# Optimization experiments

Measured on AMD Instinct MI355X. Metric: run time of the kernel, lower is better.

## Reference

```python
import jax, jax.numpy as jnp
import numpy as np
from jax.scipy.special import gammaln, xlogy

B, N, DIM, H, DK, DV = 2, 2048, 1536, 8, 64, 64
NRPF = 192  # num_rel_pos_features, already divisible by 6


def get_positional_embed(n, feat):
    # Enformer positional basis: exponential, central-mask, gamma; then sign-antisymmetrized.
    nb = feat // 6  # num basis per class
    d = jnp.arange(-n + 1, n, dtype=jnp.float32)          # [2n-1]
    ad = jnp.abs(d)[:, None]                              # [2n-1, 1]
    # exponential decay features
    max_range = np.log(n) / np.log(2.0)
    half_life = 2.0 ** jnp.linspace(3.0, max_range, nb)
    e = jnp.exp(-np.log(2.0) / half_life * ad)
    # central mask features
    widths = 2.0 ** jnp.arange(1, nb + 1, dtype=jnp.float32) - 1.0
    c = (widths > ad).astype(jnp.float32)
    # gamma pdf features
    std = n / (2.0 * nb)
    mean = jnp.linspace(n / nb, float(n), nb)
    conc = (mean / std) ** 2
    rate = mean / (std ** 2)
    logp = xlogy(conc - 1.0, ad) - rate * ad - (gammaln(conc) - conc * jnp.log(rate))
    p = jnp.exp(logp) + 1e-8
    g = p / jnp.max(p)
    emb = jnp.concatenate([e, c, g], axis=-1)             # [2n-1, feat//2]
    return jnp.concatenate([emb, jnp.sign(d)[:, None] * emb], axis=-1)  # [2n-1, feat]


def relative_shift(x):
    # x: [b, h, i, 2i-1] -> [b, h, i, i]
    b, h, i, j = x.shape
    x = jnp.pad(x, ((0, 0), (0, 0), (0, 0), (1, 0)))      # [b,h,i,j+1]
    x = x.reshape(b, h, j + 1, i)[:, :, 1:, :]            # drop first 'row'
    x = x.reshape(b, h, i, j)
    return x[..., : (j + 2) // 2]                          # keep first i cols


def setup_inputs() -> dict:
    key = jax.random.key(0)
    ks = jax.random.split(key, 9)
    s = 0.02
    return {
        "x": jax.random.normal(ks[0], (B, N, DIM), jnp.float32),
        "Wq": jax.random.normal(ks[1], (DIM, H * DK), jnp.float32) * s,
        "Wk": jax.random.normal(ks[2], (DIM, H * DK), jnp.float32) * s,
        "Wv": jax.random.normal(ks[3], (DIM, H * DV), jnp.float32) * s,
        "Wo": jax.random.normal(ks[4], (H * DV, DIM), jnp.float32) * s,
        "bo": jnp.zeros((DIM,), jnp.float32),
        "Wrel": jax.random.normal(ks[5], (NRPF, H * DK), jnp.float32) * s,
        "rel_content_bias": jax.random.normal(ks[6], (1, H, 1, DK), jnp.float32),
        "rel_pos_bias": jax.random.normal(ks[7], (1, H, 1, DK), jnp.float32),
    }


def reference(x, Wq, Wk, Wv, Wo, bo, Wrel, rel_content_bias, rel_pos_bias):
    b, n, _ = x.shape
    scale = DK ** -0.5
    split = lambda t, d: t.reshape(b, n, H, d).transpose(0, 2, 1, 3)  # b h n d
    q = split(x @ Wq, DK) * scale
    k = split(x @ Wk, DK)
    v = split(x @ Wv, DV)
    content_logits = jnp.einsum('bhid,bhjd->bhij', q + rel_content_bias, k)
    pos = get_positional_embed(n, NRPF) @ Wrel               # [2n-1, H*DK]
    pos = pos.reshape(2 * n - 1, H, DK).transpose(1, 0, 2)   # h j d
    rel_logits = jnp.einsum('bhid,hjd->bhij', q + rel_pos_bias, pos)
    rel_logits = relative_shift(rel_logits)
    attn = jax.nn.softmax(content_logits + rel_logits, axis=-1)
    out = jnp.einsum('bhij,bhjd->bhid', attn, v)
    out = out.transpose(0, 2, 1, 3).reshape(b, n, H * DV)
    return out @ Wo + bo
```

## Files before the change

### kernel.cpp

```cpp
#include <hip/hip_runtime.h>
#include <stdint.h>
#include <cmath>

#define B_    2
#define N_    2048
#define DIM_  1536
#define H_    8
#define NPOS  (2*N_ - 1)
#define NB_   32

typedef __attribute__((ext_vector_type(8))) short short8;
typedef __attribute__((ext_vector_type(4))) float float4v;

struct PosConsts {
    float  inv_hl[32];
    int    widthI[32];
    float  c1[32];
    float  rateF[32];
    double gc[32];
    double maxp;
};

__device__ __forceinline__ float bf2f(unsigned short u) {
    return __uint_as_float(((unsigned int)u) << 16);
}
__device__ __forceinline__ unsigned short f2bf(float f) {
    unsigned int u = __float_as_uint(f);
    u += 0x7FFFu + ((u >> 16) & 1u);
    return (unsigned short)(u >> 16);
}
__device__ __forceinline__ unsigned int cvtpk(float lo, float hi) {
    unsigned int r;
    asm("v_cvt_pk_bf16_f32 %0, %1, %2" : "=v"(r) : "v"(lo), "v"(hi));
    return r;
}
__device__ __forceinline__ unsigned int pack2bf(float lo, float hi) {
    return cvtpk(lo, hi);
}
__device__ __forceinline__ float ldf(const void* p, int isF32, size_t idx) {
    return isF32 ? ((const float*)p)[idx] : bf2f(((const unsigned short*)p)[idx]);
}
__device__ __forceinline__ void gll16(const unsigned short* g, unsigned short* l) {
    __builtin_amdgcn_global_load_lds(
        (const __attribute__((address_space(1))) unsigned int*)g,
        (__attribute__((address_space(3))) unsigned int*)l, 16, 0, 0);
}

constexpr size_t OFF_FLAG = 0;
constexpr size_t OFF_POS  = 256;
constexpr size_t OFF_Q    = OFF_POS + (size_t)H_*4096*64*2;
constexpr size_t OFF_K    = OFF_Q   + (size_t)B_*H_*N_*64*2;
constexpr size_t OFF_V    = OFF_K   + (size_t)B_*H_*N_*64*2;
constexpr size_t OFF_WOT  = OFF_V   + (size_t)B_*H_*N_*64*2;
constexpr size_t OFF_XB   = OFF_WOT + (size_t)DIM_*512*2;
constexpr size_t OFF_AO   = OFF_XB;
constexpr size_t OFF_OP   = OFF_AO + (size_t)4096*512*2;
constexpr size_t OFF_LP   = OFF_OP + (size_t)3*16*32*4096*2;
constexpr size_t OFF_WT   = OFF_XB + (size_t)4096*DIM_*2;
static_assert(OFF_LP + (size_t)3*16*32*64*4 <= OFF_WT + (size_t)3*512*DIM_*2, "ws overflow");

__global__ __launch_bounds__(512) void prep_kernel(PosConsts pc,
                                                   const void* __restrict__ x,
                                                   const void* __restrict__ Wq, const void* __restrict__ Wk,
                                                   const void* __restrict__ Wv, const void* __restrict__ Wo,
                                                   const void* __restrict__ Wrel,
                                                   unsigned int* __restrict__ flags,
                                                   unsigned short* __restrict__ Xb,
                                                   unsigned short* __restrict__ Wt,
                                                   unsigned short* __restrict__ Wot,
                                                   unsigned short* __restrict__ posb) {
    __shared__ __align__(16) char smraw[16 * 192 * 4];
    const int tid = threadIdx.x;
    const int bid = blockIdx.x;

    int* cnt = (int*)smraw;
    int ok = 0;
    if (tid < 256) {
        unsigned short u = ((const unsigned short*)x)[2 * tid];
        int e = (u >> 7) & 0xFF;
        ok = (u == 0) || (e >= 95 && e <= 140);
    }
    cnt[tid] = ok;
    __syncthreads();
    for (int s = 256; s > 0; s >>= 1) {
        if (tid < s) cnt[tid] += cnt[tid + s];
        __syncthreads();
    }
    const int f32 = !(cnt[0] >= 192);
    __syncthreads();
    if (bid == 0 && tid == 0) flags[0] = (unsigned int)f32;

    if (bid < 256) {
        float* eb = (float*)smraw;
        const int j0 = bid * 16;
        const int c  = tid;
        for (int u = c; u < 16 * 96; u += 512) {
            int rr = u / 96, f = u - rr * 96;
            int j = j0 + rr;
            float v = 0.f, sg = 0.f;
            if (j < NPOS) {
                int dd  = j - (N_ - 1);
                int adI = dd < 0 ? -dd : dd;
                float val;
                if (f < 32) {
                    val = exp2f(-(float)adI * pc.inv_hl[f]);
                } else if (f < 64) {
                    val = (adI < pc.widthI[f - 32]) ? 1.f : 0.f;
                } else {
                    int g = f - 64;
                    if (adI == 0) {
                        val = (float)(1e-8 / pc.maxp);
                    } else {
                        double lp = (double)pc.c1[g] * log((double)adI)
                                  - (double)pc.rateF[g] * (double)adI + pc.gc[g];
                        double p = (double)expf((float)lp) + 1e-8;
                        val = (float)(p / pc.maxp);
                    }
                }
                v  = val;
                sg = (dd > 0) ? 1.f : ((dd < 0) ? -1.f : 0.f);
            }
            eb[rr * 192 + f]      = v;
            eb[rr * 192 + 96 + f] = sg * v;
        }
        __syncthreads();
        float acc[16];
#pragma unroll
        for (int rr = 0; rr < 16; ++rr) acc[rr] = 0.f;
        for (int k = 0; k < 192; k += 4) {
            float w0 = ldf(Wrel, f32, (size_t)(k + 0) * 512 + c);
            float w1 = ldf(Wrel, f32, (size_t)(k + 1) * 512 + c);
            float w2 = ldf(Wrel, f32, (size_t)(k + 2) * 512 + c);
            float w3 = ldf(Wrel, f32, (size_t)(k + 3) * 512 + c);
#pragma unroll
            for (int rr = 0; rr < 16; ++rr) {
                float4v e = *reinterpret_cast<const float4v*>(&eb[rr * 192 + k]);
                acc[rr] += e[0] * w0;
                acc[rr] += e[1] * w1;
                acc[rr] += e[2] * w2;
                acc[rr] += e[3] * w3;
            }
        }
        int h = c >> 6, dcol = c & 63;
#pragma unroll
        for (int rr = 0; rr < 16; ++rr) {
            int j = j0 + rr;
            if (j < NPOS)
                posb[((size_t)h * 4096 + j) * 64 + dcol] = f2bf(acc[rr]);
        }
    } else if (bid < 3328) {
        unsigned short (*tile)[33] = (unsigned short(*)[33])smraw;
        const int idx = bid - 256;
        const int z = idx / 768, rem = idx % 768;
        const int bx = rem & 15, by = rem >> 4;
        const void* src = z == 0 ? Wq : (z == 1 ? Wk : (z == 2 ? Wv : Wo));
        unsigned short* dst = (z < 3) ? (Wt + (size_t)z * 512 * DIM_) : Wot;
        const int R = (z < 3) ? DIM_ : 512;
        const int C = (z < 3) ? 512 : DIM_;
        const int x0 = ((z < 3) ? bx : by) * 32;
        const int y0 = ((z < 3) ? by : bx) * 32;
        const int tx = tid & 31, ty = tid >> 5;
#pragma unroll
        for (int i = 0; i < 2; ++i)
            tile[ty + i * 16][tx] = f2bf(ldf(src, f32, (size_t)(y0 + ty + i * 16) * C + x0 + tx));
        __syncthreads();
#pragma unroll
        for (int i = 0; i < 2; ++i)
            dst[(size_t)(x0 + ty + i * 16) * R + y0 + tx] = tile[tx][ty + i * 16];
    } else {
        const int ab = bid - 3328;
        const size_t total = (size_t)4096 * DIM_;
        size_t i = ((size_t)ab * 512 + tid) * 8;
        const size_t stride = (size_t)1024 * 512 * 8;
        if (f32) {
            for (; i < total; i += stride) {
                float4v a = *reinterpret_cast<const float4v*>((const float*)x + i);
                float4v b = *reinterpret_cast<const float4v*>((const float*)x + i + 4);
                uint4 o;
                o.x = pack2bf(a[0], a[1]); o.y = pack2bf(a[2], a[3]);
                o.z = pack2bf(b[0], b[1]); o.w = pack2bf(b[2], b[3]);
                *reinterpret_cast<uint4*>(Xb + i) = o;
            }
        } else {
            for (; i < total; i += stride)
                *reinterpret_cast<uint4*>(Xb + i) =
                    *reinterpret_cast<const uint4*>((const unsigned short*)x + i);
        }
    }
}

__device__ __forceinline__ void gemm128_core(const unsigned short* __restrict__ A,
                                             const unsigned short* __restrict__ Bt,
                                             int K, int row0, int col0,
                                             unsigned short* As, unsigned short* Bs,
                                             float4v acc[4][4]) {
    const int tid = threadIdx.x, lane = tid & 63, w = tid >> 6;
    const int l15 = lane & 15, q8 = (lane >> 4) * 8;
    const int mr0 = (w >> 1) * 64, nc0 = (w & 1) * 64;
    const int sr = lane >> 2, sc8 = (lane & 3) * 8;
    for (int k0 = 0; k0 < K; k0 += 32) {
        __syncthreads();
        gll16(&A [(size_t)(row0 + w * 32 + sr) * K + k0 + sc8],      &As[w * 1024]);
        gll16(&A [(size_t)(row0 + w * 32 + 16 + sr) * K + k0 + sc8], &As[w * 1024 + 512]);
        gll16(&Bt[(size_t)(col0 + w * 32 + sr) * K + k0 + sc8],      &Bs[w * 1024]);
        gll16(&Bt[(size_t)(col0 + w * 32 + 16 + sr) * K + k0 + sc8], &Bs[w * 1024 + 512]);
        __syncthreads();
        short8 a[4], b[4];
#pragma unroll
        for (int mi = 0; mi < 4; ++mi)
            a[mi] = *reinterpret_cast<const short8*>(&As[(mr0 + mi * 16 + l15) * 32 + q8]);
#pragma unroll
        for (int ni = 0; ni < 4; ++ni)
            b[ni] = *reinterpret_cast<const short8*>(&Bs[(nc0 + ni * 16 + l15) * 32 + q8]);
#pragma unroll
        for (int mi = 0; mi < 4; ++mi)
#pragma unroll
            for (int ni = 0; ni < 4; ++ni)
                acc[mi][ni] = __builtin_amdgcn_mfma_f32_16x16x32_bf16(a[mi], b[ni], acc[mi][ni], 0, 0, 0);
    }
}

__global__ __launch_bounds__(256) void qkv_kernel(const unsigned short* __restrict__ Xb,
                                                  const unsigned short* __restrict__ Wt,
                                                  unsigned short* __restrict__ qbuf,
                                                  unsigned short* __restrict__ kbuf,
                                                  unsigned short* __restrict__ vbuf) {
    __shared__ __align__(16) unsigned short As[128 * 32];
    __shared__ __align__(16) unsigned short Bs[128 * 32];
    const int row0 = blockIdx.y * 128, col0 = blockIdx.x * 128;
    float4v acc[4][4];
#pragma unroll
    for (int mi = 0; mi < 4; ++mi)
#pragma unroll
        for (int ni = 0; ni < 4; ++ni) acc[mi][ni] = (float4v){0.f, 0.f, 0.f, 0.f};
    gemm128_core(Xb, Wt, DIM_, row0, col0, As, Bs, acc);
    const int lane = threadIdx.x & 63, w = threadIdx.x >> 6;
    const int l15 = lane & 15, quad = lane >> 4;
    const int mr0 = (w >> 1) * 64, nc0 = (w & 1) * 64;
#pragma unroll
    for (int mi = 0; mi < 4; ++mi)
#pragma unroll
        for (int ni = 0; ni < 4; ++ni) {
            int n = col0 + nc0 + ni * 16 + l15;
            int mode = n >> 9, nn = n & 511;
            int hh = nn >> 6, dd = nn & 63;
            int mb = row0 + mr0 + mi * 16 + quad * 4;
            int bb = mb >> 11, ii = mb & 2047;
            if (mode == 2) {
                union { unsigned short us[4]; uint2 u2; } pk;
                unsigned int p0 = cvtpk(acc[mi][ni][0], acc[mi][ni][1]);
                unsigned int p1 = cvtpk(acc[mi][ni][2], acc[mi][ni][3]);
                pk.u2 = (uint2){p0, p1};
                *reinterpret_cast<uint2*>(
                    &vbuf[((size_t)(bb * 8 + hh) * 64 + dd) * 2048 + ii]) = pk.u2;
            } else {
                unsigned short* Obuf = (mode == 0) ? qbuf : kbuf;
                float scale = (mode == 0) ? 0.125f : 1.0f;
#pragma unroll
                for (int r = 0; r < 4; ++r)
                    Obuf[((size_t)(bb * 8 + hh) * N_ + ii + r) * 64 + dd] = f2bf(acc[mi][ni][r] * scale);
            }
        }
}

#define SLD 72
#define RST 68

__device__ __forceinline__ void stage64(const unsigned short* __restrict__ g,
                                        unsigned short* __restrict__ s, int tid) {
    int r = tid >> 2, d0 = (tid & 3) * 16;
    const uint4* p = reinterpret_cast<const uint4*>(g + (size_t)r * 64 + d0);
    *reinterpret_cast<uint4*>(&s[r * SLD + d0])     = p[0];
    *reinterpret_cast<uint4*>(&s[r * SLD + d0 + 8]) = p[1];
}

__global__ __launch_bounds__(256) void attn_kernel(const unsigned int* __restrict__ flags,
                                                   const unsigned short* __restrict__ qb,
                                                   const unsigned short* __restrict__ kb,
                                                   const unsigned short* __restrict__ vb,
                                                   const unsigned short* __restrict__ posb,
                                                   const void* __restrict__ rcb,
                                                   const void* __restrict__ rpb,
                                                   unsigned short* __restrict__ Opart,
                                                   float* __restrict__ lpart) {
    __shared__ __align__(16) unsigned short Ks[64 * SLD];
    __shared__ __align__(16) unsigned short Ps[64 * SLD];
    __shared__ __align__(16) unsigned short Vt[64 * SLD];
    __shared__ __align__(16) unsigned short Pp[64 * SLD];
    __shared__ __align__(8)  unsigned short Rb[128 * RST];

    const int f32 = (int)flags[0];
    const int tid = threadIdx.x;
    const int it = blockIdx.x, bh = blockIdx.y, z = blockIdx.z;
    const int h = bh & 7;
    const int i0 = it * 64;
    const size_t qoff = (size_t)bh * N_ * 64;
    const size_t voff = (size_t)bh * 64 * 2048;
    const size_t poff = (size_t)h * 4096 * 64;
    const int lane = tid & 63, w = tid >> 6;
    const int l15 = lane & 15, quad = lane >> 4, q8 = quad * 8;
    const int m0 = w * 16 + quad * 4;
    const int sr = tid >> 2, sc = (tid & 3) * 16;

    short8 afc[2], afr[2];
#pragma unroll
    for (int kc = 0; kc < 2; ++kc) {
        uint4 qv = *reinterpret_cast<const uint4*>(
            &qb[qoff + (size_t)(i0 + w * 16 + l15) * 64 + kc * 32 + q8]);
        unsigned int uu[4] = {qv.x, qv.y, qv.z, qv.w};
        unsigned int cw[4], rw[4];
#pragma unroll
        for (int e = 0; e < 4; ++e) {
            int k = h * 64 + kc * 32 + q8 + 2 * e;
            float lo = __uint_as_float(uu[e] << 16);
            float hi = __uint_as_float(uu[e] & 0xffff0000u);
            cw[e] = pack2bf(lo + ldf(rcb, f32, k), hi + ldf(rcb, f32, k + 1));
            rw[e] = pack2bf(lo + ldf(rpb, f32, k), hi + ldf(rpb, f32, k + 1));
        }
        union { uint4 u; short8 s; } cv, rv2;
        cv.u  = (uint4){cw[0], cw[1], cw[2], cw[3]};
        rv2.u = (uint4){rw[0], rw[1], rw[2], rw[3]};
        afc[kc] = cv.s;
        afr[kc] = rv2.s;
    }

    float4v Oa[4];
#pragma unroll
    for (int nb = 0; nb < 4; ++nb) Oa[nb] = (float4v){0.f, 0.f, 0.f, 0.f};
    float lsum[4] = {0.f, 0.f, 0.f, 0.f};

    const int base0 = 1984 - i0;
    const int t0 = z * 11, t1 = (z == 2) ? 32 : (t0 + 11);
    const int cs0 = base0 + t0 * 64;

    stage64(&posb[poff + (size_t)cs0 * 64], Ps, tid);
    __syncthreads();
    {
        float4v R[4];
#pragma unroll
        for (int nb = 0; nb < 4; ++nb) R[nb] = (float4v){0.f, 0.f, 0.f, 0.f};
        __builtin_amdgcn_s_setprio(1);
#pragma unroll
        for (int kc = 0; kc < 2; ++kc)
#pragma unroll
            for (int nb = 0; nb < 4; ++nb) {
                short8 pb = *reinterpret_cast<const short8*>(&Ps[(nb * 16 + l15) * SLD + kc * 32 + q8]);
                R[nb] = __builtin_amdgcn_mfma_f32_16x16x32_bf16(afr[kc], pb, R[nb], 0, 0, 0);
            }
        __builtin_amdgcn_s_setprio(0);
#pragma unroll
        for (int nb = 0; nb < 4; ++nb) {
            int ta = cs0 + nb * 16 + l15;
            unsigned int pk0 = cvtpk(R[nb][0], R[nb][1]);
            unsigned int pk1 = cvtpk(R[nb][2], R[nb][3]);
            Rb[(size_t)((ta + m0 + 0) & 127) * RST + m0 + 0] = (unsigned short)pk0;
            Rb[(size_t)((ta + m0 + 1) & 127) * RST + m0 + 1] = (unsigned short)(pk0 >> 16);
            Rb[(size_t)((ta + m0 + 2) & 127) * RST + m0 + 2] = (unsigned short)pk1;
            Rb[(size_t)((ta + m0 + 3) & 127) * RST + m0 + 3] = (unsigned short)(pk1 >> 16);
        }
    }
    __syncthreads();

    stage64(&kb[qoff + (size_t)(t0 * 64) * 64], Ks, tid);
    stage64(&posb[poff + (size_t)(cs0 + 64) * 64], Ps, tid);
    {
        const unsigned short* gv = &vb[voff + (size_t)sr * 2048 + t0 * 64 + sc];
        *reinterpret_cast<uint4*>(&Vt[sr * SLD + sc])     = *reinterpret_cast<const uint4*>(gv);
        *reinterpret_cast<uint4*>(&Vt[sr * SLD + sc + 8]) = *reinterpret_cast<const uint4*>(gv + 8);
    }
    __syncthreads();

    for (int jt = t0; jt < t1; ++jt) {
        const int j0 = jt * 64, basej = base0 + j0;
        const bool hasn = (jt + 1 < t1);

        uint4 kr0, kr1, pr0, pr1, vr0, vr1;
        if (hasn) {
            const unsigned short* gk = &kb[qoff + (size_t)(j0 + 64 + sr) * 64 + sc];
            kr0 = *reinterpret_cast<const uint4*>(gk);
            kr1 = *reinterpret_cast<const uint4*>(gk + 8);
            const unsigned short* gp = &posb[poff + (size_t)(basej + 128 + sr) * 64 + sc];
            pr0 = *reinterpret_cast<const uint4*>(gp);
            pr1 = *reinterpret_cast<const uint4*>(gp + 8);
            const unsigned short* gv = &vb[voff + (size_t)sr * 2048 + j0 + 64 + sc];
            vr0 = *reinterpret_cast<const uint4*>(gv);
            vr1 = *reinterpret_cast<const uint4*>(gv + 8);
            __builtin_amdgcn_sched_barrier(0);
        }

        {
            float4v R[4];
#pragma unroll
            for (int nb = 0; nb < 4; ++nb) R[nb] = (float4v){0.f, 0.f, 0.f, 0.f};
            __builtin_amdgcn_s_setprio(1);
#pragma unroll
            for (int kc = 0; kc < 2; ++kc)
#pragma unroll
                for (int nb = 0; nb < 4; ++nb) {
                    short8 pb = *reinterpret_cast<const short8*>(&Ps[(nb * 16 + l15) * SLD + kc * 32 + q8]);
                    R[nb] = __builtin_amdgcn_mfma_f32_16x16x32_bf16(afr[kc], pb, R[nb], 0, 0, 0);
                }
            __builtin_amdgcn_s_setprio(0);
            const int tb = basej + 64;
#pragma unroll
            for (int nb = 0; nb < 4; ++nb) {
                int ta = tb + nb * 16 + l15;
                unsigned int pk0 = cvtpk(R[nb][0], R[nb][1]);
                unsigned int pk1 = cvtpk(R[nb][2], R[nb][3]);
                Rb[(size_t)((ta + m0 + 0) & 127) * RST + m0 + 0] = (unsigned short)pk0;
                Rb[(size_t)((ta + m0 + 1) & 127) * RST + m0 + 1] = (unsigned short)(pk0 >> 16);
                Rb[(size_t)((ta + m0 + 2) & 127) * RST + m0 + 2] = (unsigned short)pk1;
                Rb[(size_t)((ta + m0 + 3) & 127) * RST + m0 + 3] = (unsigned short)(pk1 >> 16);
            }
        }

        float4v Sacc[4];
#pragma unroll
        for (int nb = 0; nb < 4; ++nb) Sacc[nb] = (float4v){0.f, 0.f, 0.f, 0.f};
        __builtin_amdgcn_s_setprio(1);
#pragma unroll
        for (int kc = 0; kc < 2; ++kc)
#pragma unroll
            for (int nb = 0; nb < 4; ++nb) {
                short8 kf = *reinterpret_cast<const short8*>(&Ks[(nb * 16 + l15) * SLD + kc * 32 + q8]);
                Sacc[nb] = __builtin_amdgcn_mfma_f32_16x16x32_bf16(afc[kc], kf, Sacc[nb], 0, 0, 0);
            }
        __builtin_amdgcn_s_setprio(0);

        float pv4[4][4];
#pragma unroll
        for (int nb = 0; nb < 4; ++nb) {
            const int jl = nb * 16 + l15;
            const int row = (basej + 63 + jl) & 127;
            union { uint2 u2; unsigned short us[4]; } rv;
            rv.u2 = *reinterpret_cast<const uint2*>(&Rb[(size_t)row * RST + m0]);
#pragma unroll
            for (int r = 0; r < 4; ++r) {
                float p = __expf(Sacc[nb][r] + bf2f(rv.us[r]));
                pv4[nb][r] = p;
                lsum[r] += p;
            }
        }
#pragma unroll
        for (int r = 0; r < 4; ++r) {
            unsigned short* prow = &Pp[(m0 + r) * SLD + l15];
#pragma unroll
            for (int np = 0; np < 2; ++np) {
                unsigned int pk = cvtpk(pv4[2 * np][r], pv4[2 * np + 1][r]);
                prow[(2 * np) * 16]     = (unsigned short)pk;
                prow[(2 * np + 1) * 16] = (unsigned short)(pk >> 16);
            }
        }

        __builtin_amdgcn_s_setprio(1);
#pragma unroll
        for (int kc = 0; kc < 2; ++kc) {
            short8 pf = *reinterpret_cast<const short8*>(&Pp[(w * 16 + l15) * SLD + kc * 32 + q8]);
#pragma unroll
            for (int nb = 0; nb < 4; ++nb) {
                short8 vf = *reinterpret_cast<const short8*>(&Vt[(nb * 16 + l15) * SLD + kc * 32 + q8]);
                Oa[nb] = __builtin_amdgcn_mfma_f32_16x16x32_bf16(pf, vf, Oa[nb], 0, 0, 0);
            }
        }
        __builtin_amdgcn_s_setprio(0);

        if (hasn) {
            __syncthreads();
            *reinterpret_cast<uint4*>(&Ks[sr * SLD + sc])     = kr0;
            *reinterpret_cast<uint4*>(&Ks[sr * SLD + sc + 8]) = kr1;
            *reinterpret_cast<uint4*>(&Ps[sr * SLD + sc])     = pr0;
            *reinterpret_cast<uint4*>(&Ps[sr * SLD + sc + 8]) = pr1;
            *reinterpret_cast<uint4*>(&Vt[sr * SLD + sc])     = vr0;
            *reinterpret_cast<uint4*>(&Vt[sr * SLD + sc + 8]) = vr1;
            __syncthreads();
        }
    }

#pragma unroll
    for (int r = 0; r < 4; ++r)
#pragma unroll
        for (int off = 1; off < 16; off <<= 1) lsum[r] += __shfl_xor(lsum[r], off);
    const size_t pslot = (size_t)(z * 16 + bh) * 32 + it;
    const size_t obase = pslot * 4096;
#pragma unroll
    for (int nb = 0; nb < 4; ++nb) {
        unsigned int pk0 = cvtpk(Oa[nb][0], Oa[nb][1]);
        unsigned int pk1 = cvtpk(Oa[nb][2], Oa[nb][3]);
        unsigned short* prow = &Pp[m0 * SLD + nb * 16 + l15];
        prow[0 * SLD] = (unsigned short)pk0;
        prow[1 * SLD] = (unsigned short)(pk0 >> 16);
        prow[2 * SLD] = (unsigned short)pk1;
        prow[3 * SLD] = (unsigned short)(pk1 >> 16);
    }
    {
        const int rr2 = w * 16 + (lane >> 2), cc2 = (lane & 3) * 16;
        uint4 o0 = *reinterpret_cast<const uint4*>(&Pp[rr2 * SLD + cc2]);
        uint4 o1 = *reinterpret_cast<const uint4*>(&Pp[rr2 * SLD + cc2 + 8]);
        *reinterpret_cast<uint4*>(&Opart[obase + (size_t)rr2 * 64 + cc2])     = o0;
        *reinterpret_cast<uint4*>(&Opart[obase + (size_t)rr2 * 64 + cc2 + 8]) = o1;
    }
    if (l15 == 0) {
#pragma unroll
        for (int r = 0; r < 4; ++r) lpart[pslot * 64 + m0 + r] = lsum[r];
    }
}

__global__ __launch_bounds__(256) void combine_kernel(const unsigned short* __restrict__ Opart,
                                                      const float* __restrict__ lpart,
                                                      unsigned short* __restrict__ ao) {
    const int it = blockIdx.x, bh = blockIdx.y;
    const int h = bh & 7, b = bh >> 3, i0 = it * 64;
    const int tid = threadIdx.x;
    const int row = tid >> 2, c0 = (tid & 3) * 16;
    float o[16];
#pragma unroll
    for (int e = 0; e < 16; ++e) o[e] = 0.f;
    float l = 0.f;
#pragma unroll
    for (int z = 0; z < 3; ++z) {
        const size_t pslot = (size_t)(z * 16 + bh) * 32 + it;
        const size_t ob = pslot * 4096 + (size_t)row * 64 + c0;
        uint4 a = *reinterpret_cast<const uint4*>(&Opart[ob]);
        uint4 b4 = *reinterpret_cast<const uint4*>(&Opart[ob + 8]);
        unsigned int uu[8] = {a.x, a.y, a.z, a.w, b4.x, b4.y, b4.z, b4.w};
#pragma unroll
        for (int e = 0; e < 8; ++e) {
            o[2 * e]     += __uint_as_float(uu[e] << 16);
            o[2 * e + 1] += __uint_as_float(uu[e] & 0xffff0000u);
        }
        l += lpart[pslot * 64 + row];
    }
    float inv = 1.0f / l;
    unsigned int ou[8];
#pragma unroll
    for (int e = 0; e < 8; ++e) ou[e] = pack2bf(o[2 * e] * inv, o[2 * e + 1] * inv);
    unsigned short* dst = &ao[((size_t)b * N_ + i0 + row) * 512 + h * 64 + c0];
    *reinterpret_cast<uint4*>(dst)     = (uint4){ou[0], ou[1], ou[2], ou[3]};
    *reinterpret_cast<uint4*>(dst + 8) = (uint4){ou[4], ou[5], ou[6], ou[7]};
}

__global__ __launch_bounds__(256) void outproj_kernel(const unsigned int* __restrict__ flags,
                                                      const unsigned short* __restrict__ AO,
                                                      const unsigned short* __restrict__ Wot,
                                                      const void* __restrict__ bo,
                                                      void* __restrict__ out) {
    __shared__ __align__(16) unsigned short As[128 * 32];
    __shared__ __align__(16) unsigned short Bs[128 * 32];
    const int f32 = (int)flags[0];
    const int row0 = blockIdx.y * 128, col0 = blockIdx.x * 128;
    float4v acc[4][4];
#pragma unroll
    for (int mi = 0; mi < 4; ++mi)
#pragma unroll
        for (int ni = 0; ni < 4; ++ni) acc[mi][ni] = (float4v){0.f, 0.f, 0.f, 0.f};
    gemm128_core(AO, Wot, 512, row0, col0, As, Bs, acc);
    const int lane = threadIdx.x & 63, w = threadIdx.x >> 6;
    const int l15 = lane & 15, quad = lane >> 4;
    const int mr0 = (w >> 1) * 64, nc0 = (w & 1) * 64;
#pragma unroll
    for (int mi = 0; mi < 4; ++mi)
#pragma unroll
        for (int ni = 0; ni < 4; ++ni) {
            int n = col0 + nc0 + ni * 16 + l15;
            float bias = ldf(bo, f32, n);
#pragma unroll
            for (int r = 0; r < 4; ++r) {
                int m = row0 + mr0 + mi * 16 + quad * 4 + r;
                float v = acc[mi][ni][r] + bias;
                if (f32) ((float*)out)[(size_t)m * DIM_ + n] = v;
                else     ((unsigned short*)out)[(size_t)m * DIM_ + n] = f2bf(v);
            }
        }
}

extern "C" void kernel_launch(void* const* d_in, const int* in_sizes, int n_in,
                              void* d_out, int out_size, void* d_ws, size_t ws_size,
                              hipStream_t stream) {
    const void* x    = d_in[0];
    const void* Wq   = d_in[1];
    const void* Wk   = d_in[2];
    const void* Wv   = d_in[3];
    const void* Wo   = d_in[4];
    const void* bo   = d_in[5];
    const void* Wrel = d_in[6];
    const void* rcb  = d_in[7];
    const void* rpb  = d_in[8];

    char* ws = (char*)d_ws;
    unsigned int*   flags = (unsigned int*)(ws + OFF_FLAG);
    unsigned short* posb  = (unsigned short*)(ws + OFF_POS);
    unsigned short* qbuf  = (unsigned short*)(ws + OFF_Q);
    unsigned short* kbuf  = (unsigned short*)(ws + OFF_K);
    unsigned short* vbuf  = (unsigned short*)(ws + OFF_V);
    unsigned short* Wot   = (unsigned short*)(ws + OFF_WOT);
    unsigned short* Xb    = (unsigned short*)(ws + OFF_XB);
    unsigned short* ao    = (unsigned short*)(ws + OFF_AO);
    unsigned short* Opart = (unsigned short*)(ws + OFF_OP);
    float*          lpart = (float*)(ws + OFF_LP);
    unsigned short* Wt    = (unsigned short*)(ws + OFF_WT);

    PosConsts pc;
    double maxp = 0.0;
    for (int g = 0; g < NB_; ++g) {
        double mean = 64.0 * (g + 1);
        double conc = (mean / 32.0) * (mean / 32.0);
        double rate = mean / 1024.0;
        double lgc  = std::lgamma(conc);
        double clr  = conc * std::log(rate);
        for (int ad = 1; ad < N_; ++ad) {
            double lp = (conc - 1.0) * std::log((double)ad) - rate * (double)ad - lgc + clr;
            double p  = std::exp(lp) + 1e-8;
            if (p > maxp) maxp = p;
        }
        pc.c1[g]    = (float)(conc - 1.0);
        pc.rateF[g] = (float)rate;
        pc.gc[g]    = -lgc + clr;
    }
    pc.maxp = maxp;
    const double max_range = std::log((double)N_) / std::log(2.0);
    for (int f = 0; f < 32; ++f) {
        double t = 3.0 + (double)f * (max_range - 3.0) / 31.0;
        pc.inv_hl[f] = (float)std::exp2(-t);
        int e = f + 1;
        pc.widthI[f] = (e >= 12) ? 0x7FFFFFFF : ((1 << e) - 1);
    }

    prep_kernel<<<dim3(4352), dim3(512), 0, stream>>>(pc, x, Wq, Wk, Wv, Wo, Wrel,
                                                      flags, Xb, Wt, Wot, posb);
    qkv_kernel<<<dim3(12, 32), dim3(256), 0, stream>>>(Xb, Wt, qbuf, kbuf, vbuf);
    attn_kernel<<<dim3(32, 16, 3), dim3(256), 0, stream>>>(flags, qbuf, kbuf, vbuf, posb, rcb, rpb, Opart, lpart);
    combine_kernel<<<dim3(32, 16), dim3(256), 0, stream>>>(Opart, lpart, ao);
    outproj_kernel<<<dim3(12, 32), dim3(256), 0, stream>>>(flags, ao, Wot, bo, d_out);
}
```

Before: 263.4 us.

## Double-buffer attention K/pos/V tiles with direct global-to-LDS loads and XOR swizzle

Replaces the register-staged single-buffer K, positional and V tiles in the attention loop with double-buffered LDS tiles filled by direct global-to-LDS loads (gll16), prefetching the next tile while the current one is computed. The producers of K, V and the positional table now write in an XOR-swizzled layout, so the unpadded 64-wide LDS rows avoid bank conflicts when MFMA fragments are read. This removes one of the two barriers per iteration and the register round-trip, but doubles LDS use for these buffers. It also relies on gll16 ordering, with only one barrier per iteration ordering the async loads.

```diff
diff --git a/kernel.cpp b/kernel.cpp
--- a/kernel.cpp
+++ b/kernel.cpp
@@ -146,7 +146,7 @@
         for (int rr = 0; rr < 16; ++rr) {
             int j = j0 + rr;
             if (j < NPOS)
-                posb[((size_t)h * 4096 + j) * 64 + dcol] = f2bf(acc[rr]);
+                posb[((size_t)h * 4096 + j) * 64 + (dcol ^ ((j & 7) << 3))] = f2bf(acc[rr]);
         }
     } else if (bid < 3328) {
         unsigned short (*tile)[33] = (unsigned short(*)[33])smraw;
@@ -251,14 +251,20 @@
                 unsigned int p0 = cvtpk(acc[mi][ni][0], acc[mi][ni][1]);
                 unsigned int p1 = cvtpk(acc[mi][ni][2], acc[mi][ni][3]);
                 pk.u2 = (uint2){p0, p1};
+                int jb = (ii & ~63) | ((ii & 63) ^ ((dd & 7) << 3));
                 *reinterpret_cast<uint2*>(
-                    &vbuf[((size_t)(bb * 8 + hh) * 64 + dd) * 2048 + ii]) = pk.u2;
+                    &vbuf[((size_t)(bb * 8 + hh) * 64 + dd) * 2048 + jb]) = pk.u2;
+            } else if (mode == 1) {
+#pragma unroll
+                for (int r = 0; r < 4; ++r) {
+                    int tok = ii + r;
+                    kbuf[((size_t)(bb * 8 + hh) * N_ + tok) * 64 + (dd ^ ((tok & 7) << 3))]
+                        = f2bf(acc[mi][ni][r]);
+                }
             } else {
-                unsigned short* Obuf = (mode == 0) ? qbuf : kbuf;
-                float scale = (mode == 0) ? 0.125f : 1.0f;
 #pragma unroll
                 for (int r = 0; r < 4; ++r)
-                    Obuf[((size_t)(bb * 8 + hh) * N_ + ii + r) * 64 + dd] = f2bf(acc[mi][ni][r] * scale);
+                    qbuf[((size_t)(bb * 8 + hh) * N_ + ii + r) * 64 + dd] = f2bf(acc[mi][ni][r] * 0.125f);
             }
         }
 }
@@ -266,12 +272,21 @@
 #define SLD 72
 #define RST 68
 
-__device__ __forceinline__ void stage64(const unsigned short* __restrict__ g,
-                                        unsigned short* __restrict__ s, int tid) {
-    int r = tid >> 2, d0 = (tid & 3) * 16;
-    const uint4* p = reinterpret_cast<const uint4*>(g + (size_t)r * 64 + d0);
-    *reinterpret_cast<uint4*>(&s[r * SLD + d0])     = p[0];
-    *reinterpret_cast<uint4*>(&s[r * SLD + d0 + 8]) = p[1];
+__device__ __forceinline__ void stage_lin(const unsigned short* __restrict__ g,
+                                          unsigned short* s, int tid, int w) {
+    gll16(g + tid * 8,        s + w * 512);
+    gll16(g + 2048 + tid * 8, s + 2048 + w * 512);
+}
+__device__ __forceinline__ void stage_vt(const unsigned short* __restrict__ vbase,
+                                         int jbase, unsigned short* s, int tid, int w) {
+    {
+        int L = tid * 8;        int d = L >> 6, cb = L & 63;
+        gll16(vbase + (size_t)d * 2048 + jbase + cb, s + w * 512);
+    }
+    {
+        int L = 2048 + tid * 8; int d = L >> 6, cb = L & 63;
+        gll16(vbase + (size_t)d * 2048 + jbase + cb, s + 2048 + w * 512);
+    }
 }
 
 __global__ __launch_bounds__(256) void attn_kernel(const unsigned int* __restrict__ flags,
@@ -283,9 +298,9 @@
                                                    const void* __restrict__ rpb,
                                                    unsigned short* __restrict__ Opart,
                                                    float* __restrict__ lpart) {
-    __shared__ __align__(16) unsigned short Ks[64 * SLD];
-    __shared__ __align__(16) unsigned short Ps[64 * SLD];
-    __shared__ __align__(16) unsigned short Vt[64 * SLD];
+    __shared__ __align__(16) unsigned short Ks[2][4096];
+    __shared__ __align__(16) unsigned short Ps[2][4096];
+    __shared__ __align__(16) unsigned short Vt[2][4096];
     __shared__ __align__(16) unsigned short Pp[64 * SLD];
     __shared__ __align__(8)  unsigned short Rb[128 * RST];
 
@@ -295,12 +310,12 @@
     const int h = bh & 7;
     const int i0 = it * 64;
     const size_t qoff = (size_t)bh * N_ * 64;
-    const size_t voff = (size_t)bh * 64 * 2048;
     const size_t poff = (size_t)h * 4096 * 64;
+    const unsigned short* vbase = vb + (size_t)bh * 64 * 2048;
     const int lane = tid & 63, w = tid >> 6;
     const int l15 = lane & 15, quad = lane >> 4, q8 = quad * 8;
     const int m0 = w * 16 + quad * 4;
-    const int sr = tid >> 2, sc = (tid & 3) * 16;
+    const int swz = (l15 & 7) << 3;
 
     short8 afc[2], afr[2];
 #pragma unroll
@@ -331,9 +346,15 @@
 
     const int base0 = 1984 - i0;
     const int t0 = z * 11, t1 = (z == 2) ? 32 : (t0 + 11);
+    const int NT = t1 - t0;
     const int cs0 = base0 + t0 * 64;
 
-    stage64(&posb[poff + (size_t)cs0 * 64], Ps, tid);
+    {
+        int r = tid >> 2, c16 = (tid & 3) * 16;
+        const uint4* psrc = reinterpret_cast<const uint4*>(&posb[poff + (size_t)(cs0 + r) * 64 + c16]);
+        *reinterpret_cast<uint4*>(&Ps[0][r * 64 + c16])     = psrc[0];
+        *reinterpret_cast<uint4*>(&Ps[0][r * 64 + c16 + 8]) = psrc[1];
+    }
     __syncthreads();
     {
         float4v R[4];
@@ -344,7 +365,8 @@
         for (int kc = 0; kc < 2; ++kc)
 #pragma unroll
             for (int nb = 0; nb < 4; ++nb) {
-                short8 pb = *reinterpret_cast<const short8*>(&Ps[(nb * 16 + l15) * SLD + kc * 32 + q8]);
+                short8 pb = *reinterpret_cast<const short8*>(
+                    &Ps[0][(nb * 16 + l15) * 64 + ((kc * 32 + q8) ^ swz)]);
                 R[nb] = __builtin_amdgcn_mfma_f32_16x16x32_bf16(afr[kc], pb, R[nb], 0, 0, 0);
             }
         __builtin_amdgcn_s_setprio(0);
@@ -361,31 +383,19 @@
     }
     __syncthreads();
 
-    stage64(&kb[qoff + (size_t)(t0 * 64) * 64], Ks, tid);
-    stage64(&posb[poff + (size_t)(cs0 + 64) * 64], Ps, tid);
-    {
-        const unsigned short* gv = &vb[voff + (size_t)sr * 2048 + t0 * 64 + sc];
-        *reinterpret_cast<uint4*>(&Vt[sr * SLD + sc])     = *reinterpret_cast<const uint4*>(gv);
-        *reinterpret_cast<uint4*>(&Vt[sr * SLD + sc + 8]) = *reinterpret_cast<const uint4*>(gv + 8);
-    }
-    __syncthreads();
-
-    for (int jt = t0; jt < t1; ++jt) {
-        const int j0 = jt * 64, basej = base0 + j0;
-        const bool hasn = (jt + 1 < t1);
-
-        uint4 kr0, kr1, pr0, pr1, vr0, vr1;
-        if (hasn) {
-            const unsigned short* gk = &kb[qoff + (size_t)(j0 + 64 + sr) * 64 + sc];
-            kr0 = *reinterpret_cast<const uint4*>(gk);
-            kr1 = *reinterpret_cast<const uint4*>(gk + 8);
-            const unsigned short* gp = &posb[poff + (size_t)(basej + 128 + sr) * 64 + sc];
-            pr0 = *reinterpret_cast<const uint4*>(gp);
-            pr1 = *reinterpret_cast<const uint4*>(gp + 8);
-            const unsigned short* gv = &vb[voff + (size_t)sr * 2048 + j0 + 64 + sc];
-            vr0 = *reinterpret_cast<const uint4*>(gv);
-            vr1 = *reinterpret_cast<const uint4*>(gv + 8);
-            __builtin_amdgcn_sched_barrier(0);
+    stage_lin(&kb[qoff + (size_t)(t0 * 64) * 64], Ks[0], tid, w);
+    stage_lin(&posb[poff + (size_t)(cs0 + 64) * 64], Ps[0], tid, w);
+    stage_vt(vbase, t0 * 64, Vt[0], tid, w);
+
+    for (int u = 0; u < NT; ++u) {
+        const int p = u & 1;
+        const int j0 = (t0 + u) * 64, basej = base0 + j0;
+        __syncthreads();
+
+        if (u + 1 < NT) {
+            stage_lin(&kb[qoff + (size_t)(j0 + 64) * 64], Ks[p ^ 1], tid, w);
+            stage_lin(&posb[poff + (size_t)(cs0 + (u + 2) * 64) * 64], Ps[p ^ 1], tid, w);
+            stage_vt(vbase, j0 + 64, Vt[p ^ 1], tid, w);
         }
 
         {
@@ -397,7 +407,8 @@
             for (int kc = 0; kc < 2; ++kc)
 #pragma unroll
                 for (int nb = 0; nb < 4; ++nb) {
-                    short8 pb = *reinterpret_cast<const short8*>(&Ps[(nb * 16 + l15) * SLD + kc * 32 + q8]);
+                    short8 pb = *reinterpret_cast<const short8*>(
+                        &Ps[p][(nb * 16 + l15) * 64 + ((kc * 32 + q8) ^ swz)]);
                     R[nb] = __builtin_amdgcn_mfma_f32_16x16x32_bf16(afr[kc], pb, R[nb], 0, 0, 0);
                 }
             __builtin_amdgcn_s_setprio(0);
@@ -422,7 +433,8 @@
         for (int kc = 0; kc < 2; ++kc)
 #pragma unroll
             for (int nb = 0; nb < 4; ++nb) {
-                short8 kf = *reinterpret_cast<const short8*>(&Ks[(nb * 16 + l15) * SLD + kc * 32 + q8]);
+                short8 kf = *reinterpret_cast<const short8*>(
+                    &Ks[p][(nb * 16 + l15) * 64 + ((kc * 32 + q8) ^ swz)]);
                 Sacc[nb] = __builtin_amdgcn_mfma_f32_16x16x32_bf16(afc[kc], kf, Sacc[nb], 0, 0, 0);
             }
         __builtin_amdgcn_s_setprio(0);
@@ -436,9 +448,9 @@
             rv.u2 = *reinterpret_cast<const uint2*>(&Rb[(size_t)row * RST + m0]);
 #pragma unroll
             for (int r = 0; r < 4; ++r) {
-                float p = __expf(Sacc[nb][r] + bf2f(rv.us[r]));
-                pv4[nb][r] = p;
-                lsum[r] += p;
+                float p2 = __expf(Sacc[nb][r] + bf2f(rv.us[r]));
+                pv4[nb][r] = p2;
+                lsum[r] += p2;
             }
         }
 #pragma unroll
@@ -458,22 +470,12 @@
             short8 pf = *reinterpret_cast<const short8*>(&Pp[(w * 16 + l15) * SLD + kc * 32 + q8]);
 #pragma unroll
             for (int nb = 0; nb < 4; ++nb) {
-                short8 vf = *reinterpret_cast<const short8*>(&Vt[(nb * 16 + l15) * SLD + kc * 32 + q8]);
+                short8 vf = *reinterpret_cast<const short8*>(
+                    &Vt[p][(nb * 16 + l15) * 64 + ((kc * 32 + q8) ^ swz)]);
                 Oa[nb] = __builtin_amdgcn_mfma_f32_16x16x32_bf16(pf, vf, Oa[nb], 0, 0, 0);
             }
         }
         __builtin_amdgcn_s_setprio(0);
-
-        if (hasn) {
-            __syncthreads();
-            *reinterpret_cast<uint4*>(&Ks[sr * SLD + sc])     = kr0;
-            *reinterpret_cast<uint4*>(&Ks[sr * SLD + sc + 8]) = kr1;
-            *reinterpret_cast<uint4*>(&Ps[sr * SLD + sc])     = pr0;
-            *reinterpret_cast<uint4*>(&Ps[sr * SLD + sc + 8]) = pr1;
-            *reinterpret_cast<uint4*>(&Vt[sr * SLD + sc])     = vr0;
-            *reinterpret_cast<uint4*>(&Vt[sr * SLD + sc + 8]) = vr1;
-            __syncthreads();
-        }
     }
 
 #pragma unroll
```

New measurement: 259.6 us. No clear change (-1.5%).
